# Performance work log

Hardware: AMD Instinct MI355X
Metric: run time of the kernel (lower is better)

The kernel has to match this reference:

```python
import jax, jax.numpy as jnp
import numpy as np

B, T, V, E, H = 64, 64, 32000, 512, 1024


def setup_inputs() -> dict:
    key = jax.random.key(0)
    ks = jax.random.split(key, 12)
    s = 0.02
    return {
        "hidden": jax.random.normal(ks[0], (2, B, H), jnp.float32),
        "cell": jax.random.normal(ks[1], (2, B, H), jnp.float32),
        "captions": jax.random.randint(ks[2], (B, T), 0, V, jnp.int32),
        "embed_W": jax.random.normal(ks[3], (V, E), jnp.float32) * s,
        "W_ih0": jax.random.normal(ks[4], (4 * H, E), jnp.float32) * s,
        "W_hh0": jax.random.normal(ks[5], (4 * H, H), jnp.float32) * s,
        "b_ih0": jnp.zeros((4 * H,), jnp.float32),
        "b_hh0": jnp.zeros((4 * H,), jnp.float32),
        "W_ih1": jax.random.normal(ks[6], (4 * H, H), jnp.float32) * s,
        "W_hh1": jax.random.normal(ks[7], (4 * H, H), jnp.float32) * s,
        "b_ih1": jnp.zeros((4 * H,), jnp.float32),
        "b_hh1": jnp.zeros((4 * H,), jnp.float32),
        "Wp_voc": jax.random.normal(ks[8], (V, H), jnp.float32) * s,
        "bp_voc": jnp.zeros((V,), jnp.float32),
    }


def lstm_cell(x, h, c, W_ih, W_hh, b):
    # PyTorch gate order: input, forget, cell(g), output
    gates = x @ W_ih.T + h @ W_hh.T + b  # [B, 4H]
    i, f, g, o = jnp.split(gates, 4, axis=-1)
    i, f, o = jax.nn.sigmoid(i), jax.nn.sigmoid(f), jax.nn.sigmoid(o)
    g = jnp.tanh(g)
    c_new = f * c + i * g
    h_new = o * jnp.tanh(c_new)
    return h_new, c_new


def reference(hidden, cell, captions, embed_W, W_ih0, W_hh0, b_ih0, b_hh0,
              W_ih1, W_hh1, b_ih1, b_hh1, Wp_voc, bp_voc):
    # teacher forcing (ratio=1.0): LSTM input at step t is embed(captions[:, t-1])
    x_seq = embed_W[captions[:, :-1]]        # [B, T-1, E]
    x_seq = jnp.swapaxes(x_seq, 0, 1)        # [T-1, B, E] time-major for scan
    b0 = b_ih0 + b_hh0
    b1 = b_ih1 + b_hh1

    def step(carry, x):
        h0, c0, h1, c1 = carry
        h0, c0 = lstm_cell(x, h0, c0, W_ih0, W_hh0, b0)
        h1, c1 = lstm_cell(h0, h1, c1, W_ih1, W_hh1, b1)
        logits = h1 @ Wp_voc.T + bp_voc      # [B, V]
        return (h0, c0, h1, c1), logits

    carry = (hidden[0], cell[0], hidden[1], cell[1])
    _, logits = jax.lax.scan(step, carry, x_seq)   # [T-1, B, V]
    logits = jnp.swapaxes(logits, 0, 1)            # [B, T-1, V]
    # outputs[:, 0, :] stays zero as in the torch code
    return jnp.concatenate([jnp.zeros((logits.shape[0], 1, logits.shape[2]), logits.dtype), logits], axis=1)
```

## Files before the change

kernel.cpp:

```cpp
#include <hip/hip_runtime.h>

#define B_    64
#define T_    64
#define V_    32000
#define E_    512
#define H_    1024
#define G4_   4096
#define TS_   63
#define MROWS 4032
#define MPAD  4096
#define BH    (B_ * H_)
#define FPAD  32

typedef __attribute__((ext_vector_type(8))) short bf16x8;
typedef __attribute__((ext_vector_type(4))) float f32x4;
typedef __attribute__((ext_vector_type(4))) unsigned int uint32x4;

__device__ __forceinline__ unsigned short bfbits(float f) {
  union { float f; unsigned int u; } cv; cv.f = f;
  unsigned int u = cv.u;
  u += 0x7fffu + ((u >> 16) & 1u);
  return (unsigned short)(u >> 16);
}
__device__ __forceinline__ float bf2f(unsigned short h) {
  union { unsigned int u; float f; } cv; cv.u = ((unsigned int)h) << 16;
  return cv.f;
}
__device__ __forceinline__ float fsig(float x) { return 1.f / (1.f + __expf(-x)); }
__device__ __forceinline__ float ftanh(float x) {
  x = fminf(fmaxf(x, -10.f), 10.f);
  const float e = __expf(2.f * x);
  return (e - 1.f) / (e + 1.f);
}

__device__ __forceinline__ void store_dword_dc(void* p, unsigned int v) {
  asm volatile("global_store_dword %0, %1, off sc0 sc1" :: "v"(p), "v"(v) : "memory");
}
__device__ __forceinline__ void store_b128_dc(void* p, uint32x4 v) {
  asm volatile("global_store_dwordx4 %0, %1, off sc0 sc1" :: "v"(p), "v"(v) : "memory");
}
__device__ __forceinline__ unsigned int load_dword_dc(const void* p) {
  unsigned int v;
  asm volatile("global_load_dword %0, %1, off sc0 sc1\n\ts_waitcnt vmcnt(0)"
               : "=v"(v) : "v"(p) : "memory");
  return v;
}
__device__ __forceinline__ void store_dword_nt(void* p, float f) {
  union { float f; unsigned int u; } cv; cv.f = f;
  asm volatile("global_store_dword %0, %1, off nt" :: "v"(p), "v"(cv.u) : "memory");
}

__device__ __forceinline__ void gload16(const void* g, void* l) {
  __builtin_amdgcn_global_load_lds(
      (const __attribute__((address_space(1))) unsigned int*)g,
      (__attribute__((address_space(3))) unsigned int*)l, 16, 0, 0);
}


__global__ void k_cast4(const float4* __restrict__ s, ushort4* __restrict__ d, int n4) {
  int i = blockIdx.x * blockDim.x + threadIdx.x;
  const int st = gridDim.x * blockDim.x;
  for (; i < n4; i += st) {
    const float4 f = s[i];
    ushort4 v;
    v.x = bfbits(f.x); v.y = bfbits(f.y); v.z = bfbits(f.z); v.w = bfbits(f.w);
    d[i] = v;
  }
}

__global__ void k_castW(const float4* __restrict__ s0, const float4* __restrict__ s1,
                        const float4* __restrict__ s2, const float4* __restrict__ s3,
                        ushort4* __restrict__ d0, ushort4* __restrict__ d1,
                        ushort4* __restrict__ d2, ushort4* __restrict__ d3) {
  const int N0 = G4_ * E_ / 4, N1 = G4_ * H_ / 4;
  int i = blockIdx.x * 256 + threadIdx.x;
  const int st = gridDim.x * 256;
  for (; i < N0 + 3 * N1; i += st) {
    const float4* s; ushort4* d; int k;
    if (i < N0)            { s = s0; d = d0; k = i; }
    else if (i < N0 + N1)  { s = s1; d = d1; k = i - N0; }
    else if (i < N0 + 2*N1){ s = s2; d = d2; k = i - N0 - N1; }
    else                   { s = s3; d = d3; k = i - N0 - 2 * N1; }
    const float4 f = s[k];
    ushort4 v;
    v.x = bfbits(f.x); v.y = bfbits(f.y); v.z = bfbits(f.z); v.w = bfbits(f.w);
    d[k] = v;
  }
}

__global__ void k_bias2(const float* __restrict__ a0, const float* __restrict__ b0,
                        const float* __restrict__ a1, const float* __restrict__ b1,
                        float* __restrict__ o0, float* __restrict__ o1) {
  const int i = blockIdx.x * 256 + threadIdx.x;
  if (i < G4_) o0[i] = a0[i] + b0[i];
  else         o1[i - G4_] = a1[i - G4_] + b1[i - G4_];
}

__global__ void k_gather(const float* __restrict__ embed, const int* __restrict__ caps,
                         unsigned short* __restrict__ X) {
  const int i = blockIdx.x * 256 + threadIdx.x;
  const int m = i >> 7, e4 = i & 127;
  ushort4 v;
  if (m < MROWS) {
    const int t = m >> 6, b = m & 63;
    const int idx = caps[b * T_ + t];
    const float4 f = ((const float4*)embed)[(long)idx * (E_ / 4) + e4];
    v.x = bfbits(f.x); v.y = bfbits(f.y); v.z = bfbits(f.z); v.w = bfbits(f.w);
  } else {
    v = make_ushort4(0, 0, 0, 0);
  }
  ((ushort4*)X)[i] = v;
}

__global__ void k_init(const float* __restrict__ hidden, const float* __restrict__ cell,
                       unsigned short* __restrict__ H0, unsigned short* __restrict__ H1,
                       float* __restrict__ c0, float* __restrict__ c1,
                       unsigned int* __restrict__ flags) {
  const int i = blockIdx.x * 256 + threadIdx.x;
  if (i < B_ * H_) {
    H0[i] = bfbits(hidden[i]);
    H1[i] = bfbits(hidden[B_ * H_ + i]);
    c0[i] = cell[i];
    c1[i] = cell[B_ * H_ + i];
    if (i < 192 * FPAD) flags[i] = 0u;
  } else {
    const int j = i - B_ * H_;
    H0[(size_t)MPAD * H_ + j] = 0;
    H1[(size_t)MPAD * H_ + j] = 0;
  }
}

__global__ void k_zero_t0(float4* __restrict__ out4) {
  const int i = blockIdx.x * 256 + threadIdx.x;
  const int b = i / (V_ / 4), v = i - b * (V_ / 4);
  out4[(long)b * (T_ * V_ / 4) + v] = make_float4(0.f, 0.f, 0.f, 0.f);
}

__global__ __launch_bounds__(256) void k_gemm1(
    const unsigned short* __restrict__ A, const unsigned short* __restrict__ Bm,
    const float* __restrict__ bias, unsigned short* __restrict__ Cb) {
  __shared__ unsigned short As[128 * 32];
  __shared__ unsigned short Bs[128 * 32];
  const int tid = threadIdx.x;
  const int w = tid >> 6, l = tid & 63;
  const int wm = (w >> 1) * 64, wn = (w & 1) * 64;
  const int lr = l & 15, lk = (l >> 4) * 8;
  const long am0 = (long)blockIdx.y * 128;
  const long bn0 = (long)blockIdx.x * 128;

  const int u0 = tid, u1 = tid + 256;
  const char* gA0 = (const char*)(A + (am0 + (u0 >> 2)) * E_) + (u0 & 3) * 16;
  const char* gA1 = (const char*)(A + (am0 + (u1 >> 2)) * E_) + (u1 & 3) * 16;
  const char* gB0 = (const char*)(Bm + (bn0 + (u0 >> 2)) * E_) + (u0 & 3) * 16;
  const char* gB1 = (const char*)(Bm + (bn0 + (u1 >> 2)) * E_) + (u1 & 3) * 16;
  char* lA0 = (char*)As + u0 * 16; char* lA1 = (char*)As + u1 * 16;
  char* lB0 = (char*)Bs + u0 * 16; char* lB1 = (char*)Bs + u1 * 16;

  f32x4 acc[4][4];
  const f32x4 z = {0.f, 0.f, 0.f, 0.f};
  #pragma unroll
  for (int mi = 0; mi < 4; ++mi)
    #pragma unroll
    for (int ni = 0; ni < 4; ++ni) acc[mi][ni] = z;

  for (int k0 = 0; k0 < E_; k0 += 32) {
    __syncthreads();
    gload16(gA0 + (long)k0 * 2, lA0);
    gload16(gA1 + (long)k0 * 2, lA1);
    gload16(gB0 + (long)k0 * 2, lB0);
    gload16(gB1 + (long)k0 * 2, lB1);
    __syncthreads();
    bf16x8 af[4], bfr[4];
    #pragma unroll
    for (int mi = 0; mi < 4; ++mi)
      af[mi] = *(const bf16x8*)(As + (wm + mi * 16 + lr) * 32 + lk);
    #pragma unroll
    for (int ni = 0; ni < 4; ++ni)
      bfr[ni] = *(const bf16x8*)(Bs + (wn + ni * 16 + lr) * 32 + lk);
    #pragma unroll
    for (int mi = 0; mi < 4; ++mi)
      #pragma unroll
      for (int ni = 0; ni < 4; ++ni)
        acc[mi][ni] = __builtin_amdgcn_mfma_f32_16x16x32_bf16(af[mi], bfr[ni], acc[mi][ni], 0, 0, 0);
  }

  #pragma unroll
  for (int ni = 0; ni < 4; ++ni) {
    const int n = (int)bn0 + wn + ni * 16 + lr;
    const float bv = bias[n];
    #pragma unroll
    for (int mi = 0; mi < 4; ++mi) {
      #pragma unroll
      for (int r = 0; r < 4; ++r) {
        const int m = (int)am0 + wm + mi * 16 + (l >> 4) * 4 + r;
        Cb[(long)m * G4_ + n] = bfbits(acc[mi][ni][r] + bv);
      }
    }
  }
}

__global__ __launch_bounds__(512) void k_gemm3(
    const unsigned short* __restrict__ A,
    const unsigned short* __restrict__ Bm,
    const float* __restrict__ bias,
    float* __restrict__ out) {
  __shared__ unsigned short As[3][256 * 32];
  __shared__ unsigned short Bs[3][256 * 32];
  const int tid = threadIdx.x;
  const int wid = tid >> 6, l = tid & 63;
  const int wr = wid >> 2, wc = wid & 3;
  const int lr = l & 15, khi = l >> 4;
  const int id = blockIdx.x;
  const int by = id / 125, bx = id - by * 125;
  const long am0 = (long)by * 256;
  const long bn0 = (long)bx * 256;

  int srow[2], sq[2];
  #pragma unroll
  for (int j = 0; j < 2; ++j) {
    const int idx = j * 512 + tid;
    srow[j] = idx >> 2;
    sq[j] = (idx & 3) ^ ((srow[j] >> 1) & 3);
  }

  f32x4 acc[8][4];
  const f32x4 z = {0.f, 0.f, 0.f, 0.f};
  #pragma unroll
  for (int mf = 0; mf < 8; ++mf)
    #pragma unroll
    for (int nf = 0; nf < 4; ++nf) acc[mf][nf] = z;

  auto stage = [&](int kt, int b) {
    const long koff = (long)kt * 64;
    #pragma unroll
    for (int j = 0; j < 2; ++j) {
      const int idx = j * 512 + tid;
      gload16((const char*)(A + (am0 + srow[j]) * H_) + koff + sq[j] * 16,
              (char*)As[b] + idx * 16);
    }
    #pragma unroll
    for (int j = 0; j < 2; ++j) {
      const int idx = j * 512 + tid;
      gload16((const char*)(Bm + (bn0 + srow[j]) * H_) + koff + sq[j] * 16,
              (char*)Bs[b] + idx * 16);
    }
  };

  stage(0, 0);
  stage(1, 1);
  for (int t = 0; t < 32; ++t) {
    const int c = t % 3;
    __builtin_amdgcn_s_barrier();
    if (t + 2 < 32) {
      stage(t + 2, (t + 2) % 3);
      asm volatile("s_waitcnt vmcnt(8)" ::: "memory");
    } else if (t + 1 < 32) {
      asm volatile("s_waitcnt vmcnt(4)" ::: "memory");
    } else {
      asm volatile("s_waitcnt vmcnt(0)" ::: "memory");
    }
    __builtin_amdgcn_s_barrier();
    bf16x8 af[8], bfr[4];
    #pragma unroll
    for (int mf = 0; mf < 8; ++mf) {
      const int row = wr * 128 + mf * 16 + lr;
      const int q = khi ^ ((row >> 1) & 3);
      af[mf] = *(const bf16x8*)((const char*)As[c] + row * 64 + q * 16);
    }
    #pragma unroll
    for (int nf = 0; nf < 4; ++nf) {
      const int row = wc * 64 + nf * 16 + lr;
      const int q = khi ^ ((row >> 1) & 3);
      bfr[nf] = *(const bf16x8*)((const char*)Bs[c] + row * 64 + q * 16);
    }
    __builtin_amdgcn_s_setprio(1);
    #pragma unroll
    for (int mf = 0; mf < 8; ++mf)
      #pragma unroll
      for (int nf = 0; nf < 4; ++nf)
        acc[mf][nf] = __builtin_amdgcn_mfma_f32_16x16x32_bf16(af[mf], bfr[nf], acc[mf][nf], 0, 0, 0);
    __builtin_amdgcn_s_setprio(0);
  }

  #pragma unroll
  for (int nf = 0; nf < 4; ++nf) {
    const int n = (int)bn0 + wc * 64 + nf * 16 + lr;
    const float bv = bias[n];
    #pragma unroll
    for (int mf = 0; mf < 8; ++mf) {
      #pragma unroll
      for (int r = 0; r < 4; ++r) {
        const int m = (int)am0 + wr * 128 + mf * 16 + khi * 4 + r;
        if (m < MROWS) {
          const int t = m >> 6, b = m & 63;
          store_dword_nt(out + (long)(b * T_ + t + 1) * V_ + n, acc[mf][nf][r] + bv);
        }
      }
    }
  }
}

__global__ __launch_bounds__(256) void k_fused(
    const unsigned short* __restrict__ Whh0b,
    const unsigned short* __restrict__ Whh1b,
    const unsigned short* __restrict__ Wih1b,
    const unsigned short* __restrict__ Xp,
    unsigned short* __restrict__ H0b,
    unsigned short* __restrict__ H1b,
    const float* __restrict__ c0i, const float* __restrict__ c1i,
    const float* __restrict__ b1s,
    unsigned int* __restrict__ f0,
    unsigned int* __restrict__ f1) {
  __shared__ unsigned short Wl[64 * 1024];
  __shared__ __align__(16) float gs1[4][64][8];
  unsigned short (*hexch)[16] = (unsigned short (*)[16])gs1;

  const int tid = threadIdx.x;
  const int w = tid >> 6, l = tid & 63;
  const int lcol = l & 15, khi = l >> 4;
  const int bw = w * 16;
  const f32x4 z = {0.f, 0.f, 0.f, 0.f};

  if (blockIdx.x < 64) {
    const int blk = blockIdx.x;
    const int jb = blk << 4;
    for (int u = tid; u < 64 * 128; u += 256) {
      const int rr = u >> 7, cu = u & 127;
      const int g = rr >> 4, jj = rr & 15;
      ((bf16x8*)Wl)[rr * 128 + (cu ^ (rr & 7))] =
          *(const bf16x8*)(Whh0b + (size_t)(g * 1024 + jb + jj) * H_ + cu * 8);
    }
    f32x4 cr;
    #pragma unroll
    for (int r = 0; r < 4; ++r)
      cr[r] = c0i[(size_t)(bw + khi * 4 + r) * H_ + jb + lcol];
    unsigned short pin[16];
    #pragma unroll
    for (int r = 0; r < 4; ++r) {
      const unsigned short* ir = Xp + (size_t)(bw + khi * 4 + r) * G4_ + jb + lcol;
      pin[r * 4 + 0] = ir[0];
      pin[r * 4 + 1] = ir[H_];
      pin[r * 4 + 2] = ir[2 * H_];
      pin[r * 4 + 3] = ir[3 * H_];
    }
    __syncthreads();

    for (int s = 0; s < TS_; ++s) {
      if (s > 0) {
        if (tid < 64)
          while (load_dword_dc(&f0[tid << 5]) < (unsigned)s) __builtin_amdgcn_s_sleep(1);
        __syncthreads();
      }
      f32x4 a0, a1, a2, a3;
      #pragma unroll
      for (int r = 0; r < 4; ++r) {
        a0[r] = bf2f(pin[r * 4 + 0]);
        a1[r] = bf2f(pin[r * 4 + 1]);
        a2[r] = bf2f(pin[r * 4 + 2]);
        a3[r] = bf2f(pin[r * 4 + 3]);
      }
      const unsigned short* hrow = H0b + (size_t)s * BH + (size_t)(bw + lcol) * H_ + khi * 8;
      #pragma unroll 8
      for (int kk = 0; kk < 32; ++kk) {
        const bf16x8 av = *(const bf16x8*)(hrow + kk * 32);
        const int un = (kk * 4 + khi) ^ (lcol & 7);
        const bf16x8 b0 = ((const bf16x8*)Wl)[(0 * 16 + lcol) * 128 + un];
        const bf16x8 b1 = ((const bf16x8*)Wl)[(1 * 16 + lcol) * 128 + un];
        const bf16x8 b2 = ((const bf16x8*)Wl)[(2 * 16 + lcol) * 128 + un];
        const bf16x8 b3 = ((const bf16x8*)Wl)[(3 * 16 + lcol) * 128 + un];
        a0 = __builtin_amdgcn_mfma_f32_16x16x32_bf16(av, b0, a0, 0, 0, 0);
        a1 = __builtin_amdgcn_mfma_f32_16x16x32_bf16(av, b1, a1, 0, 0, 0);
        a2 = __builtin_amdgcn_mfma_f32_16x16x32_bf16(av, b2, a2, 0, 0, 0);
        a3 = __builtin_amdgcn_mfma_f32_16x16x32_bf16(av, b3, a3, 0, 0, 0);
      }
      #pragma unroll
      for (int r = 0; r < 4; ++r) {
        const float gi = fsig(a0[r]);
        const float gf = fsig(a1[r]);
        const float gg = ftanh(a2[r]);
        const float go = fsig(a3[r]);
        cr[r] = gf * cr[r] + gi * gg;
        hexch[bw + khi * 4 + r][lcol] = bfbits(go * ftanh(cr[r]));
      }
      if (s + 1 < TS_) {
        const unsigned short* inb = Xp + (size_t)(s + 1) * (B_ * G4_);
        #pragma unroll
        for (int r = 0; r < 4; ++r) {
          const unsigned short* ir = inb + (size_t)(bw + khi * 4 + r) * G4_ + jb + lcol;
          pin[r * 4 + 0] = ir[0];
          pin[r * 4 + 1] = ir[H_];
          pin[r * 4 + 2] = ir[2 * H_];
          pin[r * 4 + 3] = ir[3 * H_];
        }
      }
      __syncthreads();
      if (tid < 128) {
        const int b = tid >> 1, hf = tid & 1;
        const uint32x4 v = *(const uint32x4*)&hexch[b][hf * 8];
        store_b128_dc(H0b + (size_t)(s + 1) * BH + (size_t)b * H_ + jb + hf * 8, v);
      }
      __syncthreads();
      if (tid == 0) store_dword_dc(&f0[blk << 5], (unsigned)(s + 1));
    }
  } else {
    const int blk1 = blockIdx.x - 64;
    const int jb1 = blk1 << 3;
    for (int u = tid; u < 64 * 128; u += 256) {
      const int pr = u >> 7, cu = u & 127;
      const int prl = pr & 31, tt = prl >> 4, lr_ = prl & 15;
      const int g = tt * 2 + (lr_ >> 3), jj = lr_ & 7;
      const unsigned short* src =
          ((pr >> 5) ? Wih1b : Whh1b) + (size_t)(g * 1024 + jb1 + jj) * H_ + cu * 8;
      ((bf16x8*)Wl)[pr * 128 + (cu ^ (pr & 7))] = *(const bf16x8*)src;
    }
    const int bb = tid >> 2;
    const int j0 = (tid * 2) & 7;
    float cA = c1i[(size_t)bb * H_ + jb1 + j0];
    float cB = c1i[(size_t)bb * H_ + jb1 + j0 + 1];
    float biA[4], biB[4];
    #pragma unroll
    for (int g = 0; g < 4; ++g) {
      biA[g] = b1s[g * 1024 + jb1 + j0];
      biB[g] = b1s[g * 1024 + jb1 + j0 + 1];
    }
    __syncthreads();

    for (int s = 1; s <= TS_; ++s) {
      {
        const unsigned t0 = (unsigned)s, t1 = (unsigned)(s - 1);
        if (tid < 64) {
          while (load_dword_dc(&f0[tid << 5]) < t0) __builtin_amdgcn_s_sleep(1);
        } else if (tid < 192) {
          while (load_dword_dc(&f1[(tid - 64) << 5]) < t1) __builtin_amdgcn_s_sleep(1);
        }
        __syncthreads();
      }
      f32x4 ac0 = z, ac1 = z;
      const unsigned short* a1p = H1b + (size_t)(s - 1) * BH + (size_t)(bw + lcol) * H_ + khi * 8;
      const unsigned short* a0p = H0b + (size_t)s * BH + (size_t)(bw + lcol) * H_ + khi * 8;
      #pragma unroll 8
      for (int kk = 0; kk < 32; ++kk) {
        const bf16x8 av = *(const bf16x8*)(a1p + kk * 32);
        const int un = (kk * 4 + khi) ^ (lcol & 7);
        const bf16x8 b0 = ((const bf16x8*)Wl)[(0 + lcol) * 128 + un];
        const bf16x8 b1 = ((const bf16x8*)Wl)[(16 + lcol) * 128 + un];
        ac0 = __builtin_amdgcn_mfma_f32_16x16x32_bf16(av, b0, ac0, 0, 0, 0);
        ac1 = __builtin_amdgcn_mfma_f32_16x16x32_bf16(av, b1, ac1, 0, 0, 0);
      }
      #pragma unroll 8
      for (int kk = 0; kk < 32; ++kk) {
        const bf16x8 av = *(const bf16x8*)(a0p + kk * 32);
        const int un = (kk * 4 + khi) ^ (lcol & 7);
        const bf16x8 b0 = ((const bf16x8*)Wl)[(32 + lcol) * 128 + un];
        const bf16x8 b1 = ((const bf16x8*)Wl)[(48 + lcol) * 128 + un];
        ac0 = __builtin_amdgcn_mfma_f32_16x16x32_bf16(av, b0, ac0, 0, 0, 0);
        ac1 = __builtin_amdgcn_mfma_f32_16x16x32_bf16(av, b1, ac1, 0, 0, 0);
      }
      #pragma unroll
      for (int r = 0; r < 4; ++r) {
        const int b = bw + khi * 4 + r;
        gs1[lcol >> 3][b][lcol & 7] = ac0[r];
        gs1[2 + (lcol >> 3)][b][lcol & 7] = ac1[r];
      }
      __syncthreads();
      {
        const float giA = fsig(gs1[0][bb][j0] + biA[0]);
        const float gfA = fsig(gs1[1][bb][j0] + biA[1]);
        const float ggA = ftanh(gs1[2][bb][j0] + biA[2]);
        const float goA = fsig(gs1[3][bb][j0] + biA[3]);
        cA = gfA * cA + giA * ggA;
        const unsigned short hA = bfbits(goA * ftanh(cA));
        const float giB = fsig(gs1[0][bb][j0 + 1] + biB[0]);
        const float gfB = fsig(gs1[1][bb][j0 + 1] + biB[1]);
        const float ggB = ftanh(gs1[2][bb][j0 + 1] + biB[2]);
        const float goB = fsig(gs1[3][bb][j0 + 1] + biB[3]);
        cB = gfB * cB + giB * ggB;
        const unsigned short hB = bfbits(goB * ftanh(cB));
        const unsigned int hv = ((unsigned int)hB << 16) | hA;
        store_dword_dc(H1b + (size_t)s * BH + (size_t)bb * H_ + jb1 + j0, hv);
      }
      __syncthreads();
      if (tid == 0) store_dword_dc(&f1[blk1 << 5], (unsigned)s);
    }
  }
}


extern "C" void kernel_launch(void* const* d_in, const int* in_sizes, int n_in,
                              void* d_out, int out_size, void* d_ws, size_t ws_size,
                              hipStream_t stream) {
  (void)in_sizes; (void)n_in; (void)out_size; (void)ws_size;
  const float* hidden = (const float*)d_in[0];
  const float* cell   = (const float*)d_in[1];
  const int*   caps   = (const int*)d_in[2];
  const float* embed  = (const float*)d_in[3];
  const float* Wih0   = (const float*)d_in[4];
  const float* Whh0   = (const float*)d_in[5];
  const float* bih0   = (const float*)d_in[6];
  const float* bhh0   = (const float*)d_in[7];
  const float* Wih1   = (const float*)d_in[8];
  const float* Whh1   = (const float*)d_in[9];
  const float* bih1   = (const float*)d_in[10];
  const float* bhh1   = (const float*)d_in[11];
  const float* Wp     = (const float*)d_in[12];
  const float* bp     = (const float*)d_in[13];
  float* out = (float*)d_out;

  char* p = (char*)d_ws;
  auto alloc = [&](size_t bytes) { char* r = p; p += (bytes + 255) & ~(size_t)255; return r; };
  unsigned short* Xbf   = (unsigned short*)alloc((size_t)MPAD * E_ * 2);
  unsigned short* Wih0b = (unsigned short*)alloc((size_t)G4_ * E_ * 2);
  unsigned short* Whh0b = (unsigned short*)alloc((size_t)G4_ * H_ * 2);
  unsigned short* Wih1b = (unsigned short*)alloc((size_t)G4_ * H_ * 2);
  unsigned short* Whh1b = (unsigned short*)alloc((size_t)G4_ * H_ * 2);
  unsigned short* Wpb   = (unsigned short*)alloc((size_t)V_ * H_ * 2);
  unsigned short* Xp    = (unsigned short*)alloc((size_t)MPAD * G4_ * 2);
  unsigned short* H0    = (unsigned short*)alloc((size_t)(MPAD + B_) * H_ * 2);
  unsigned short* H1    = (unsigned short*)alloc((size_t)(MPAD + B_) * H_ * 2);
  float* c0  = (float*)alloc((size_t)B_ * H_ * 4);
  float* c1  = (float*)alloc((size_t)B_ * H_ * 4);
  float* b0s = (float*)alloc((size_t)G4_ * 4);
  float* b1s = (float*)alloc((size_t)G4_ * 4);
  unsigned int* cbar = (unsigned int*)alloc((size_t)192 * FPAD * 4);

  k_castW<<<4096, 256, 0, stream>>>((const float4*)Wih0, (const float4*)Whh0,
                                    (const float4*)Wih1, (const float4*)Whh1,
                                    (ushort4*)Wih0b, (ushort4*)Whh0b,
                                    (ushort4*)Wih1b, (ushort4*)Whh1b);
  k_cast4<<<4096, 256, 0, stream>>>((const float4*)Wp, (ushort4*)Wpb, V_ * H_ / 4);
  k_bias2<<<32, 256, 0, stream>>>(bih0, bhh0, bih1, bhh1, b0s, b1s);
  k_gather<<<2048, 256, 0, stream>>>(embed, caps, Xbf);
  k_init<<<512, 256, 0, stream>>>(hidden, cell, H0, H1, c0, c1, cbar);
  k_zero_t0<<<2000, 256, 0, stream>>>((float4*)out);

  k_gemm1<<<dim3(32, 32), 256, 0, stream>>>(Xbf, Wih0b, b0s, Xp);

  k_fused<<<192, 256, 0, stream>>>(Whh0b, Whh1b, Wih1b, Xp, H0, H1, c0, c1, b1s,
                                   cbar, cbar + 64 * FPAD);

  k_gemm3<<<2000, 512, 0, stream>>>(H1 + (size_t)B_ * H_, Wpb, bp, out);
}
```

Measured before the change: 1.085 ms.

## Retile input-projection GEMM to 256x256 and deepen K-step to 64

k_gemm1 moves from a 128x128 tile with a single LDS buffer to a 256x256 tile, 512 threads, a double-buffered pipeline and an XOR-swizzled LDS layout, matching the vocab GEMM's structure. k_gemm3 switches from a triple buffer with K-step 32 to a double buffer with K-step 64, halving the number of barriers per tile. The aim is fewer sync points and more MFMA work between them. In exchange, LDS per block reaches 128KB with less prefetch depth, and k_gemm1 now launches only 256 blocks.

```diff
diff --git a/kernel.cpp b/kernel.cpp
--- a/kernel.cpp
+++ b/kernel.cpp
@@ -136,76 +136,108 @@
   out4[(long)b * (T_ * V_ / 4) + v] = make_float4(0.f, 0.f, 0.f, 0.f);
 }
 
-__global__ __launch_bounds__(256) void k_gemm1(
-    const unsigned short* __restrict__ A, const unsigned short* __restrict__ Bm,
-    const float* __restrict__ bias, unsigned short* __restrict__ Cb) {
-  __shared__ unsigned short As[128 * 32];
-  __shared__ unsigned short Bs[128 * 32];
+__global__ __launch_bounds__(512, 2) void k_gemm1(
+    const unsigned short* __restrict__ A,
+    const unsigned short* __restrict__ Bm,
+    const float* __restrict__ bias,
+    unsigned short* __restrict__ Cb) {
+  __shared__ unsigned short As[2][256 * 64];
+  __shared__ unsigned short Bs[2][256 * 64];
   const int tid = threadIdx.x;
-  const int w = tid >> 6, l = tid & 63;
-  const int wm = (w >> 1) * 64, wn = (w & 1) * 64;
-  const int lr = l & 15, lk = (l >> 4) * 8;
-  const long am0 = (long)blockIdx.y * 128;
-  const long bn0 = (long)blockIdx.x * 128;
-
-  const int u0 = tid, u1 = tid + 256;
-  const char* gA0 = (const char*)(A + (am0 + (u0 >> 2)) * E_) + (u0 & 3) * 16;
-  const char* gA1 = (const char*)(A + (am0 + (u1 >> 2)) * E_) + (u1 & 3) * 16;
-  const char* gB0 = (const char*)(Bm + (bn0 + (u0 >> 2)) * E_) + (u0 & 3) * 16;
-  const char* gB1 = (const char*)(Bm + (bn0 + (u1 >> 2)) * E_) + (u1 & 3) * 16;
-  char* lA0 = (char*)As + u0 * 16; char* lA1 = (char*)As + u1 * 16;
-  char* lB0 = (char*)Bs + u0 * 16; char* lB1 = (char*)Bs + u1 * 16;
-
-  f32x4 acc[4][4];
+  const int wid = tid >> 6, l = tid & 63;
+  const int wr = wid >> 2, wc = wid & 3;
+  const int lr = l & 15, khi = l >> 4;
+  const long am0 = (long)blockIdx.y * 256;
+  const long bn0 = (long)blockIdx.x * 256;
+
+  int srow[4], sq[4];
+  #pragma unroll
+  for (int j = 0; j < 4; ++j) {
+    const int idx = j * 512 + tid;
+    srow[j] = idx >> 3;
+    sq[j] = (idx & 7) ^ (srow[j] & 7);
+  }
+
+  f32x4 acc[8][4];
   const f32x4 z = {0.f, 0.f, 0.f, 0.f};
   #pragma unroll
-  for (int mi = 0; mi < 4; ++mi)
-    #pragma unroll
-    for (int ni = 0; ni < 4; ++ni) acc[mi][ni] = z;
-
-  for (int k0 = 0; k0 < E_; k0 += 32) {
-    __syncthreads();
-    gload16(gA0 + (long)k0 * 2, lA0);
-    gload16(gA1 + (long)k0 * 2, lA1);
-    gload16(gB0 + (long)k0 * 2, lB0);
-    gload16(gB1 + (long)k0 * 2, lB1);
-    __syncthreads();
-    bf16x8 af[4], bfr[4];
-    #pragma unroll
-    for (int mi = 0; mi < 4; ++mi)
-      af[mi] = *(const bf16x8*)(As + (wm + mi * 16 + lr) * 32 + lk);
-    #pragma unroll
-    for (int ni = 0; ni < 4; ++ni)
-      bfr[ni] = *(const bf16x8*)(Bs + (wn + ni * 16 + lr) * 32 + lk);
-    #pragma unroll
-    for (int mi = 0; mi < 4; ++mi)
-      #pragma unroll
-      for (int ni = 0; ni < 4; ++ni)
-        acc[mi][ni] = __builtin_amdgcn_mfma_f32_16x16x32_bf16(af[mi], bfr[ni], acc[mi][ni], 0, 0, 0);
+  for (int mf = 0; mf < 8; ++mf)
+    #pragma unroll
+    for (int nf = 0; nf < 4; ++nf) acc[mf][nf] = z;
+
+  auto stage = [&](int kt, int b) {
+    const long koff = (long)kt * 128;
+    #pragma unroll
+    for (int j = 0; j < 4; ++j) {
+      const int idx = j * 512 + tid;
+      gload16((const char*)(A + (am0 + srow[j]) * E_) + koff + sq[j] * 16,
+              (char*)As[b] + idx * 16);
+    }
+    #pragma unroll
+    for (int j = 0; j < 4; ++j) {
+      const int idx = j * 512 + tid;
+      gload16((const char*)(Bm + (bn0 + srow[j]) * E_) + koff + sq[j] * 16,
+              (char*)Bs[b] + idx * 16);
+    }
+  };
+
+  stage(0, 0);
+  for (int t = 0; t < 8; ++t) {
+    const int c = t & 1;
+    __builtin_amdgcn_s_barrier();
+    if (t + 1 < 8) {
+      stage(t + 1, c ^ 1);
+      asm volatile("s_waitcnt vmcnt(8)" ::: "memory");
+    } else {
+      asm volatile("s_waitcnt vmcnt(0)" ::: "memory");
+    }
+    __builtin_amdgcn_s_barrier();
+    #pragma unroll
+    for (int ks = 0; ks < 2; ++ks) {
+      const int qx = ((ks * 4 + khi) ^ (lr & 7)) * 16;
+      bf16x8 af[8], bfr[4];
+      #pragma unroll
+      for (int mf = 0; mf < 8; ++mf) {
+        const int row = wr * 128 + mf * 16 + lr;
+        af[mf] = *(const bf16x8*)((const char*)As[c] + row * 128 + qx);
+      }
+      #pragma unroll
+      for (int nf = 0; nf < 4; ++nf) {
+        const int row = wc * 64 + nf * 16 + lr;
+        bfr[nf] = *(const bf16x8*)((const char*)Bs[c] + row * 128 + qx);
+      }
+      __builtin_amdgcn_s_setprio(1);
+      #pragma unroll
+      for (int mf = 0; mf < 8; ++mf)
+        #pragma unroll
+        for (int nf = 0; nf < 4; ++nf)
+          acc[mf][nf] = __builtin_amdgcn_mfma_f32_16x16x32_bf16(af[mf], bfr[nf], acc[mf][nf], 0, 0, 0);
+      __builtin_amdgcn_s_setprio(0);
+    }
   }
 
   #pragma unroll
-  for (int ni = 0; ni < 4; ++ni) {
-    const int n = (int)bn0 + wn + ni * 16 + lr;
+  for (int nf = 0; nf < 4; ++nf) {
+    const int n = (int)bn0 + wc * 64 + nf * 16 + lr;
     const float bv = bias[n];
     #pragma unroll
-    for (int mi = 0; mi < 4; ++mi) {
+    for (int mf = 0; mf < 8; ++mf) {
       #pragma unroll
       for (int r = 0; r < 4; ++r) {
-        const int m = (int)am0 + wm + mi * 16 + (l >> 4) * 4 + r;
-        Cb[(long)m * G4_ + n] = bfbits(acc[mi][ni][r] + bv);
-      }
-    }
-  }
-}
-
-__global__ __launch_bounds__(512) void k_gemm3(
+        const int m = (int)am0 + wr * 128 + mf * 16 + khi * 4 + r;
+        Cb[(long)m * G4_ + n] = bfbits(acc[mf][nf][r] + bv);
+      }
+    }
+  }
+}
+
+__global__ __launch_bounds__(512, 2) void k_gemm3(
     const unsigned short* __restrict__ A,
     const unsigned short* __restrict__ Bm,
     const float* __restrict__ bias,
     float* __restrict__ out) {
-  __shared__ unsigned short As[3][256 * 32];
-  __shared__ unsigned short Bs[3][256 * 32];
+  __shared__ unsigned short As[2][256 * 64];
+  __shared__ unsigned short Bs[2][256 * 64];
   const int tid = threadIdx.x;
   const int wid = tid >> 6, l = tid & 63;
   const int wr = wid >> 2, wc = wid & 3;
@@ -215,12 +247,12 @@
   const long am0 = (long)by * 256;
   const long bn0 = (long)bx * 256;
 
-  int srow[2], sq[2];
+  int srow[4], sq[4];
   #pragma unroll
-  for (int j = 0; j < 2; ++j) {
+  for (int j = 0; j < 4; ++j) {
     const int idx = j * 512 + tid;
-    srow[j] = idx >> 2;
-    sq[j] = (idx & 3) ^ ((srow[j] >> 1) & 3);
+    srow[j] = idx >> 3;
+    sq[j] = (idx & 7) ^ (srow[j] & 7);
   }
 
   f32x4 acc[8][4];
@@ -231,15 +263,15 @@
     for (int nf = 0; nf < 4; ++nf) acc[mf][nf] = z;
 
   auto stage = [&](int kt, int b) {
-    const long koff = (long)kt * 64;
-    #pragma unroll
-    for (int j = 0; j < 2; ++j) {
+    const long koff = (long)kt * 128;
+    #pragma unroll
+    for (int j = 0; j < 4; ++j) {
       const int idx = j * 512 + tid;
       gload16((const char*)(A + (am0 + srow[j]) * H_) + koff + sq[j] * 16,
               (char*)As[b] + idx * 16);
     }
     #pragma unroll
-    for (int j = 0; j < 2; ++j) {
+    for (int j = 0; j < 4; ++j) {
       const int idx = j * 512 + tid;
       gload16((const char*)(Bm + (bn0 + srow[j]) * H_) + koff + sq[j] * 16,
               (char*)Bs[b] + idx * 16);
@@ -247,39 +279,38 @@
   };
 
   stage(0, 0);
-  stage(1, 1);
-  for (int t = 0; t < 32; ++t) {
-    const int c = t % 3;
+  for (int t = 0; t < 16; ++t) {
+    const int c = t & 1;
     __builtin_amdgcn_s_barrier();
-    if (t + 2 < 32) {
-      stage(t + 2, (t + 2) % 3);
+    if (t + 1 < 16) {
+      stage(t + 1, c ^ 1);
       asm volatile("s_waitcnt vmcnt(8)" ::: "memory");
-    } else if (t + 1 < 32) {
-      asm volatile("s_waitcnt vmcnt(4)" ::: "memory");
     } else {
       asm volatile("s_waitcnt vmcnt(0)" ::: "memory");
     }
     __builtin_amdgcn_s_barrier();
-    bf16x8 af[8], bfr[4];
-    #pragma unroll
-    for (int mf = 0; mf < 8; ++mf) {
-      const int row = wr * 128 + mf * 16 + lr;
-      const int q = khi ^ ((row >> 1) & 3);
-      af[mf] = *(const bf16x8*)((const char*)As[c] + row * 64 + q * 16);
-    }
-    #pragma unroll
-    for (int nf = 0; nf < 4; ++nf) {
-      const int row = wc * 64 + nf * 16 + lr;
-      const int q = khi ^ ((row >> 1) & 3);
-      bfr[nf] = *(const bf16x8*)((const char*)Bs[c] + row * 64 + q * 16);
-    }
-    __builtin_amdgcn_s_setprio(1);
-    #pragma unroll
-    for (int mf = 0; mf < 8; ++mf)
-      #pragma unroll
-      for (int nf = 0; nf < 4; ++nf)
-        acc[mf][nf] = __builtin_amdgcn_mfma_f32_16x16x32_bf16(af[mf], bfr[nf], acc[mf][nf], 0, 0, 0);
-    __builtin_amdgcn_s_setprio(0);
+    #pragma unroll
+    for (int ks = 0; ks < 2; ++ks) {
+      const int qx = ((ks * 4 + khi) ^ (lr & 7)) * 16;
+      bf16x8 af[8], bfr[4];
+      #pragma unroll
+      for (int mf = 0; mf < 8; ++mf) {
+        const int row = wr * 128 + mf * 16 + lr;
+        af[mf] = *(const bf16x8*)((const char*)As[c] + row * 128 + qx);
+      }
+      #pragma unroll
+      for (int nf = 0; nf < 4; ++nf) {
+        const int row = wc * 64 + nf * 16 + lr;
+        bfr[nf] = *(const bf16x8*)((const char*)Bs[c] + row * 128 + qx);
+      }
+      __builtin_amdgcn_s_setprio(1);
+      #pragma unroll
+      for (int mf = 0; mf < 8; ++mf)
+        #pragma unroll
+        for (int nf = 0; nf < 4; ++nf)
+          acc[mf][nf] = __builtin_amdgcn_mfma_f32_16x16x32_bf16(af[mf], bfr[nf], acc[mf][nf], 0, 0, 0);
+      __builtin_amdgcn_s_setprio(0);
+    }
   }
 
   #pragma unroll
@@ -533,7 +564,7 @@
   k_init<<<512, 256, 0, stream>>>(hidden, cell, H0, H1, c0, c1, cbar);
   k_zero_t0<<<2000, 256, 0, stream>>>((float4*)out);
 
-  k_gemm1<<<dim3(32, 32), 256, 0, stream>>>(Xbf, Wih0b, b0s, Xp);
+  k_gemm1<<<dim3(16, 16), 512, 0, stream>>>(Xbf, Wih0b, b0s, Xp);
 
   k_fused<<<192, 256, 0, stream>>>(Whh0b, Whh1b, Wih1b, Xp, H0, H1, c0, c1, b1s,
                                    cbar, cbar + 64 * FPAD);
```

New measurement: 1.040 ms, median of 2. 4.2% less time.
